# Performance work log

Hardware: AMD Instinct MI355X
Metric: run time of the kernel (lower is better)

Reference implementation:

```python
import jax, jax.numpy as jnp
import numpy as np

N = 100000      # nodes
E = 800000      # directed edges (self-loops added in reference, PyG default)
F_IN = 16
H1, C1 = 3, 32  # conv1: heads=3, out=32 (concat -> 96)
H2, C2 = 1, 32  # conv2: heads=1, out=32
NC = 16         # n_channel
SLOPE = 0.2     # PyG GATConv default negative_slope


def setup_inputs() -> dict:
    key = jax.random.key(0)
    ks = jax.random.split(key, 12)
    s = 0.1
    return {
        "x": jax.random.normal(ks[0], (N, F_IN), jnp.float32),
        "edge_index": jax.random.randint(ks[1], (2, E), 0, N, dtype=jnp.int32),
        "W1": jax.random.normal(ks[2], (F_IN, H1 * C1), jnp.float32) * s,
        "a_src1": jax.random.normal(ks[3], (H1, C1), jnp.float32) * s,
        "a_dst1": jax.random.normal(ks[4], (H1, C1), jnp.float32) * s,
        "b1": jnp.zeros((H1 * C1,), jnp.float32),
        "W2": jax.random.normal(ks[5], (H1 * C1, H2 * C2), jnp.float32) * s,
        "a_src2": jax.random.normal(ks[6], (H2, C2), jnp.float32) * s,
        "a_dst2": jax.random.normal(ks[7], (H2, C2), jnp.float32) * s,
        "b2": jnp.zeros((H2 * C2,), jnp.float32),
        "Wf": jax.random.normal(ks[8], (C2, NC), jnp.float32) * s,
        "bf": jnp.zeros((NC,), jnp.float32),
    }


def _gat_layer(x, src, dst, W, a_s, a_d, b, heads, outc):
    # x: [N, Fin]; src/dst: [Etot]
    h = (x @ W).reshape(N, heads, outc)                        # [N, H, C]
    alpha_s = (h * a_s).sum(-1)                                # [N, H]
    alpha_d = (h * a_d).sum(-1)                                # [N, H]
    e = jax.nn.leaky_relu(alpha_s[src] + alpha_d[dst], SLOPE)  # [Etot, H]
    # scatter-softmax over edges grouped by destination node
    m = jax.ops.segment_max(e, dst, num_segments=N)            # [N, H]
    p = jnp.exp(e - m[dst])
    z = jax.ops.segment_sum(p, dst, num_segments=N)
    alpha = p / (z[dst] + 1e-16)                               # [Etot, H]
    out = jax.ops.segment_sum(h[src] * alpha[:, :, None], dst, num_segments=N)
    return out.reshape(N, heads * outc) + b


def reference(x, edge_index, W1, a_src1, a_dst1, b1, W2, a_src2, a_dst2, b2, Wf, bf):
    loops = jnp.arange(N, dtype=edge_index.dtype)  # PyG add_self_loops=True
    src = jnp.concatenate([edge_index[0], loops])
    dst = jnp.concatenate([edge_index[1], loops])
    h = jax.nn.selu(_gat_layer(x, src, dst, W1, a_src1, a_dst1, b1, H1, C1))
    h = jax.nn.selu(_gat_layer(h, src, dst, W2, a_src2, a_dst2, b2, H2, C2))
    return h @ Wf + bf
```

## Files before the change

### kernel.cpp

```cpp
#include <hip/hip_runtime.h>
#include <hip/hip_bf16.h>

#define N_NODES 100000
#define N_EDGES 800000
#define F_IN    16
#define H1      3
#define C1      32
#define F1      (H1*C1)
#define F2      32
#define NC      16
#define SLOPE       0.2f
#define SELU_SCALE  1.0507009873554805f
#define SELU_ALPHA  1.6732632423543772f

#define DEG_PAD 48

#define NSLICE        8
#define BLK_PER_SLICE 256
#define SCAT_BLKS     (NSLICE * BLK_PER_SLICE)
#define EDGES_PER_BLK (N_EDGES / BLK_PER_SLICE)
#define SLICE_NODES   (N_NODES / NSLICE)
#define XB_NB   ((N_NODES + 255) / 256)

typedef unsigned short ushort_t;

__device__ __forceinline__ ushort_t f2bf(float f) {
    unsigned u = __float_as_uint(f);
    return (ushort_t)((u + 0x7FFFu + ((u >> 16) & 1u)) >> 16);
}
__device__ __forceinline__ unsigned pack2bf(float a, float b) {
    return (unsigned)f2bf(a) | ((unsigned)f2bf(b) << 16);
}
__device__ __forceinline__ float bf_lo(unsigned u) { return __uint_as_float(u << 16); }
__device__ __forceinline__ float bf_hi(unsigned u) { return __uint_as_float(u & 0xFFFF0000u); }

__device__ __forceinline__ void unpack8(const uint4 v, float* f) {
    f[0] = bf_lo(v.x); f[1] = bf_hi(v.x);
    f[2] = bf_lo(v.y); f[3] = bf_hi(v.y);
    f[4] = bf_lo(v.z); f[5] = bf_hi(v.z);
    f[6] = bf_lo(v.w); f[7] = bf_hi(v.w);
}
__device__ __forceinline__ float selu_f(float u) {
    return u > 0.f ? SELU_SCALE * u : SELU_SCALE * SELU_ALPHA * (__expf(u) - 1.f);
}

__global__ __launch_bounds__(256) void build_k(
    const int* __restrict__ ei, const float* __restrict__ x,
    const float* __restrict__ W1, const float* __restrict__ aS1,
    const float* __restrict__ aD1,
    int* __restrict__ deg, int* __restrict__ colp,
    uint4* __restrict__ xb, float4* __restrict__ as4, float4* __restrict__ ad4)
{
    __shared__ float swv[F_IN * 6];
    const int b = blockIdx.x, t = threadIdx.x;
    if (b < SCAT_BLKS) {
        const int slice = b & 7;
        const int lo = slice * SLICE_NODES, hi = lo + SLICE_NODES;
        const int e0 = (b >> 3) * EDGES_PER_BLK;
        for (int e = e0 + t; e < e0 + EDGES_PER_BLK; e += 256) {
            const int d = ei[N_EDGES + e];
            if (d >= lo && d < hi) {
                const int s = ei[e];
                const int pos = atomicAdd(&deg[d], 1);
                if (pos < DEG_PAD) colp[d * DEG_PAD + pos] = s;
            }
        }
    } else {
        if (t < 96) {
            const int k = t / 6, j = t % 6;
            const int h = (j < 3) ? j : j - 3;
            const float* a = (j < 3) ? aS1 : aD1;
            float acc = 0.f;
#pragma unroll
            for (int c = 0; c < 32; ++c) acc += W1[k * F1 + h * 32 + c] * a[h * 32 + c];
            swv[k * 6 + j] = acc;
        }
        __syncthreads();
        const int node = (b - SCAT_BLKS) * 256 + t;
        if (node < N_NODES) {
            float xr[16];
            const float4* xp = reinterpret_cast<const float4*>(&x[(size_t)node * F_IN]);
            const float4 v0 = xp[0], v1 = xp[1], v2 = xp[2], v3 = xp[3];
            xr[0] = v0.x; xr[1] = v0.y; xr[2]  = v0.z; xr[3]  = v0.w;
            xr[4] = v1.x; xr[5] = v1.y; xr[6]  = v1.z; xr[7]  = v1.w;
            xr[8] = v2.x; xr[9] = v2.y; xr[10] = v2.z; xr[11] = v2.w;
            xr[12] = v3.x; xr[13] = v3.y; xr[14] = v3.z; xr[15] = v3.w;
            uint4 o0, o1;
            o0.x = pack2bf(xr[0], xr[1]);   o0.y = pack2bf(xr[2], xr[3]);
            o0.z = pack2bf(xr[4], xr[5]);   o0.w = pack2bf(xr[6], xr[7]);
            o1.x = pack2bf(xr[8], xr[9]);   o1.y = pack2bf(xr[10], xr[11]);
            o1.z = pack2bf(xr[12], xr[13]); o1.w = pack2bf(xr[14], xr[15]);
            xb[(size_t)node * 2]     = o0;
            xb[(size_t)node * 2 + 1] = o1;
            float sacc[3] = {0.f, 0.f, 0.f}, dacc[3] = {0.f, 0.f, 0.f};
#pragma unroll
            for (int k = 0; k < 16; ++k) {
                const float xk = xr[k];
#pragma unroll
                for (int j = 0; j < 3; ++j) {
                    sacc[j] += xk * swv[k * 6 + j];
                    dacc[j] += xk * swv[k * 6 + 3 + j];
                }
            }
            as4[node] = make_float4(sacc[0], sacc[1], sacc[2], 0.f);
            ad4[node] = make_float4(dacc[0], dacc[1], dacc[2], 0.f);
        }
    }
}

__global__ __launch_bounds__(256) void agg1_k(
    const int* __restrict__ deg, const int* __restrict__ colp,
    const uint4* __restrict__ xb,
    const float4* __restrict__ as4, const float4* __restrict__ ad4,
    float* __restrict__ xagg)
{
    const int t = threadIdx.x;
    const int node = blockIdx.x * 64 + (t >> 2);
    const int u = t & 1;
    const int v = (t >> 1) & 1;
    if (node >= N_NODES) return;
    const int base = node * DEG_PAD;
    const int dg = min(deg[node], DEG_PAD);
    const float4 adv = ad4[node];

    float acc[3][8];
#pragma unroll
    for (int h = 0; h < 3; ++h)
#pragma unroll
        for (int i = 0; i < 8; ++i) acc[h][i] = 0.f;
    float z0 = 0.f, z1 = 0.f, z2 = 0.f;
    if (v == 0) {
        const float4 a = as4[node];
        float e0 = a.x + adv.x; e0 = e0 > 0.f ? e0 : SLOPE * e0;
        float e1 = a.y + adv.y; e1 = e1 > 0.f ? e1 : SLOPE * e1;
        float e2 = a.z + adv.z; e2 = e2 > 0.f ? e2 : SLOPE * e2;
        const float p0 = __expf(e0), p1 = __expf(e1), p2 = __expf(e2);
        z0 = p0; z1 = p1; z2 = p2;
        float xf[8]; unpack8(xb[(size_t)node * 2 + u], xf);
#pragma unroll
        for (int i = 0; i < 8; ++i) {
            acc[0][i] = p0 * xf[i]; acc[1][i] = p1 * xf[i]; acc[2][i] = p2 * xf[i];
        }
    }
    int j = v; uint4 hv; float4 av;
    if (j < dg) { const int s = colp[base + j]; av = as4[s]; hv = xb[(size_t)s * 2 + u]; }
    while (j < dg) {
        const uint4 cx = hv; const float4 ca = av;
        const int jn = j + 2;
        if (jn < dg) {
            const int s = colp[base + jn];
            av = as4[s]; hv = xb[(size_t)s * 2 + u];
        }
        float e0 = ca.x + adv.x; e0 = e0 > 0.f ? e0 : SLOPE * e0;
        float e1 = ca.y + adv.y; e1 = e1 > 0.f ? e1 : SLOPE * e1;
        float e2 = ca.z + adv.z; e2 = e2 > 0.f ? e2 : SLOPE * e2;
        const float p0 = __expf(e0), p1 = __expf(e1), p2 = __expf(e2);
        z0 += p0; z1 += p1; z2 += p2;
        float xf[8]; unpack8(cx, xf);
#pragma unroll
        for (int i = 0; i < 8; ++i) {
            acc[0][i] += p0 * xf[i]; acc[1][i] += p1 * xf[i]; acc[2][i] += p2 * xf[i];
        }
        j = jn;
    }
    z0 += __shfl_xor(z0, 2); z1 += __shfl_xor(z1, 2); z2 += __shfl_xor(z2, 2);
#pragma unroll
    for (int h = 0; h < 3; ++h)
#pragma unroll
        for (int i = 0; i < 8; ++i) acc[h][i] += __shfl_xor(acc[h][i], 2);
    if (v == 0) {
        const float zi[3] = {1.f / (z0 + 1e-16f), 1.f / (z1 + 1e-16f), 1.f / (z2 + 1e-16f)};
#pragma unroll
        for (int h = 0; h < 3; ++h) {
            float* dst = &xagg[(size_t)node * 48 + h * 16 + u * 8];
            *reinterpret_cast<float4*>(dst) =
                make_float4(acc[h][0] * zi[h], acc[h][1] * zi[h], acc[h][2] * zi[h], acc[h][3] * zi[h]);
            *reinterpret_cast<float4*>(dst + 4) =
                make_float4(acc[h][4] * zi[h], acc[h][5] * zi[h], acc[h][6] * zi[h], acc[h][7] * zi[h]);
        }
    }
}

__global__ __launch_bounds__(384) void l12_k(
    const float* __restrict__ xagg, const float* __restrict__ W1,
    const float* __restrict__ b1, const float* __restrict__ W2,
    const float* __restrict__ aS2, const float* __restrict__ aD2,
    ushort_t* __restrict__ h2b, float* __restrict__ as2, float* __restrict__ ad2)
{
    __shared__ float sW1[F_IN * F1];
    __shared__ float sxa[32 * 48];
    __shared__ float sx2[32][F1 + 1];
    __shared__ float sW2[F1 * F2];
    __shared__ float swv[F1 * 2];
    const int t = threadIdx.x;
    const int node0 = blockIdx.x * 32;

    {
        const float4 w = *reinterpret_cast<const float4*>(&W1[t * 4]);
        *reinterpret_cast<float4*>(&sW1[t * 4]) = w;
        const float4 xa = reinterpret_cast<const float4*>(xagg)[(size_t)node0 * 12 + t];
        *reinterpret_cast<float4*>(&sxa[t * 4]) = xa;
        const float4 w2a = *reinterpret_cast<const float4*>(&W2[t * 4]);
        *reinterpret_cast<float4*>(&sW2[t * 4]) = w2a;
        const float4 w2b = *reinterpret_cast<const float4*>(&W2[(t + 384) * 4]);
        *reinterpret_cast<float4*>(&sW2[(t + 384) * 4]) = w2b;
    }
    if (t < 192) {
        const int k = t >> 1, j = t & 1;
        const float* a = j ? aD2 : aS2;
        float acc = 0.f;
#pragma unroll
        for (int c = 0; c < 32; ++c) acc += W2[k * F2 + c] * a[c];
        swv[k * 2 + j] = acc;
    }
    __syncthreads();

    {
        const int c = t % 96;
        const int nloc = t / 96;
        const int hc = c >> 5;
        const float bc = b1[c];
#pragma unroll
        for (int g = 0; g < 8; ++g) {
            const int n = g * 4 + nloc;
            float acc = bc;
#pragma unroll
            for (int k = 0; k < F_IN; ++k) acc += sxa[n * 48 + hc * 16 + k] * sW1[k * F1 + c];
            sx2[n][c] = selu_f(acc);
        }
    }
    __syncthreads();

    if (t < 256) {
        const int nloc = t >> 3;
        const int cq = t & 7;
        float a0 = 0.f, a1 = 0.f, a2 = 0.f, a3 = 0.f;
#pragma unroll 8
        for (int k = 0; k < F1; ++k) {
            const float xk = sx2[nloc][k];
            const float4 w = *reinterpret_cast<const float4*>(&sW2[k * F2 + cq * 4]);
            a0 += xk * w.x; a1 += xk * w.y; a2 += xk * w.z; a3 += xk * w.w;
        }
        const int node = node0 + nloc;
        uint2 o;
        o.x = pack2bf(a0, a1); o.y = pack2bf(a2, a3);
        *reinterpret_cast<uint2*>(&h2b[(size_t)node * F2 + cq * 4]) = o;
        if (cq < 2) {
            float acc = 0.f;
#pragma unroll 8
            for (int k = 0; k < F1; ++k) acc += sx2[nloc][k] * swv[k * 2 + cq];
            if (cq == 0) as2[node] = acc;
            else         ad2[node] = acc;
        }
    }
}

__global__ __launch_bounds__(256) void agg2_final_k(
    const int* __restrict__ deg, const int* __restrict__ colp,
    const ushort_t* __restrict__ hb,
    const float* __restrict__ as, const float* __restrict__ ad,
    const float* __restrict__ b2, const float* __restrict__ Wf,
    const float* __restrict__ bf, float* __restrict__ out)
{
    __shared__ float sW[F2 * NC];
    __shared__ float sx[64][33];
    const int t = threadIdx.x;
    for (int i = t; i < F2 * NC; i += 256) sW[i] = Wf[i];
    const int sub = t >> 2;
    const int u = t & 1;
    const int v = (t >> 1) & 1;
    const int node = blockIdx.x * 64 + sub;
    const bool valid = node < N_NODES;

    if (valid) {
        const int base = node * DEG_PAD;
        const int dg = min(deg[node], DEG_PAD);
        const float adv = ad[node];
        float acc[16];
#pragma unroll
        for (int i = 0; i < 16; ++i) acc[i] = 0.f;
        float z = 0.f;
        if (v == 0) {
            float e = as[node] + adv; e = e > 0.f ? e : SLOPE * e;
            const float pv = __expf(e);
            z = pv;
            const uint4* hp = reinterpret_cast<const uint4*>(&hb[(size_t)node * F2 + u * 16]);
            float xf[8];
            unpack8(hp[0], xf);
#pragma unroll
            for (int i = 0; i < 8; ++i) acc[i] = pv * xf[i];
            unpack8(hp[1], xf);
#pragma unroll
            for (int i = 0; i < 8; ++i) acc[8 + i] = pv * xf[i];
        }
        int j = v; uint4 hva, hvb; float asv;
        if (j < dg) {
            const int s = colp[base + j];
            asv = as[s];
            const uint4* hp = reinterpret_cast<const uint4*>(&hb[(size_t)s * F2 + u * 16]);
            hva = hp[0]; hvb = hp[1];
        }
        while (j < dg) {
            const uint4 ca = hva, cb = hvb; const float cas = asv;
            const int jn = j + 2;
            if (jn < dg) {
                const int s = colp[base + jn];
                asv = as[s];
                const uint4* hp = reinterpret_cast<const uint4*>(&hb[(size_t)s * F2 + u * 16]);
                hva = hp[0]; hvb = hp[1];
            }
            float e = cas + adv; e = e > 0.f ? e : SLOPE * e;
            const float pv = __expf(e);
            z += pv;
            float xf[8];
            unpack8(ca, xf);
#pragma unroll
            for (int i = 0; i < 8; ++i) acc[i] += pv * xf[i];
            unpack8(cb, xf);
#pragma unroll
            for (int i = 0; i < 8; ++i) acc[8 + i] += pv * xf[i];
            j = jn;
        }
        z += __shfl_xor(z, 2);
#pragma unroll
        for (int i = 0; i < 16; ++i) acc[i] += __shfl_xor(acc[i], 2);
        if (v == 0) {
            const float zi = 1.f / (z + 1e-16f);
#pragma unroll
            for (int i = 0; i < 16; ++i)
                sx[sub][u * 16 + i] = selu_f(acc[i] * zi + b2[u * 16 + i]);
        }
    }
    __syncthreads();
    if (valid) {
        const int c0 = (t & 3) * 4;
        float r[4];
#pragma unroll
        for (int i = 0; i < 4; ++i) r[i] = bf[c0 + i];
#pragma unroll
        for (int k = 0; k < F2; ++k) {
            const float xk = sx[sub][k];
#pragma unroll
            for (int i = 0; i < 4; ++i) r[i] += xk * sW[k * NC + c0 + i];
        }
        *reinterpret_cast<float4*>(&out[(size_t)node * NC + c0]) =
            make_float4(r[0], r[1], r[2], r[3]);
    }
}

extern "C" void kernel_launch(void* const* d_in, const int* in_sizes, int n_in,
                              void* d_out, int out_size, void* d_ws, size_t ws_size,
                              hipStream_t stream)
{
    const float* x    = (const float*)d_in[0];
    const int*   ei   = (const int*)d_in[1];
    const float* W1   = (const float*)d_in[2];
    const float* aS1  = (const float*)d_in[3];
    const float* aD1  = (const float*)d_in[4];
    const float* b1   = (const float*)d_in[5];
    const float* W2   = (const float*)d_in[6];
    const float* aS2  = (const float*)d_in[7];
    const float* aD2  = (const float*)d_in[8];
    const float* b2   = (const float*)d_in[9];
    const float* Wf   = (const float*)d_in[10];
    const float* bf   = (const float*)d_in[11];
    float* out = (float*)d_out;

    uint4*    xb   = (uint4*)d_ws;
    float4*   as4  = (float4*)(xb + (size_t)N_NODES * 2);
    float4*   ad4  = as4 + N_NODES;
    float*    xagg = (float*)(ad4 + N_NODES);
    ushort_t* h2b  = (ushort_t*)(xagg + (size_t)N_NODES * 48);
    float*    as2  = (float*)(h2b + (size_t)N_NODES * F2);
    float*    ad2  = as2 + N_NODES;
    int*      colp = (int*)(ad2 + N_NODES);
    int*      deg  = colp + (size_t)N_NODES * DEG_PAD;

    hipMemsetAsync(deg, 0, sizeof(int) * N_NODES, stream);
    build_k<<<SCAT_BLKS + XB_NB, 256, 0, stream>>>(
        ei, x, W1, aS1, aD1, deg, colp, xb, as4, ad4);
    agg1_k<<<(N_NODES + 63) / 64, 256, 0, stream>>>(deg, colp, xb, as4, ad4, xagg);
    l12_k<<<N_NODES / 32, 384, 0, stream>>>(xagg, W1, b1, W2, aS2, aD2, h2b, as2, ad2);
    agg2_final_k<<<(N_NODES + 63) / 64, 256, 0, stream>>>(
        deg, colp, h2b, as2, ad2, b2, Wf, bf, out);
}
```

Baseline: 150.5 us.

## Transpose padded adjacency per slice, store xagg in bf16, retile l12 to 64 nodes

The padded neighbor list now uses a per-slice position-major layout, so adjacent destination nodes write and read neighbor slot j at adjacent addresses. The layer-1 aggregate is stored as bf16 instead of fp32, halving that intermediate's write and read traffic at some precision cost. The fused linear kernel now handles 64 nodes per block, with register-blocked weights and two nodes per thread, and gains bounds checks. The larger shared-memory tiles may reduce occupancy.

```diff
diff --git a/kernel.cpp b/kernel.cpp
--- a/kernel.cpp
+++ b/kernel.cpp
@@ -57,12 +57,13 @@
         const int slice = b & 7;
         const int lo = slice * SLICE_NODES, hi = lo + SLICE_NODES;
         const int e0 = (b >> 3) * EDGES_PER_BLK;
+        int* cslice = colp + (size_t)slice * DEG_PAD * SLICE_NODES;
         for (int e = e0 + t; e < e0 + EDGES_PER_BLK; e += 256) {
             const int d = ei[N_EDGES + e];
             if (d >= lo && d < hi) {
                 const int s = ei[e];
                 const int pos = atomicAdd(&deg[d], 1);
-                if (pos < DEG_PAD) colp[d * DEG_PAD + pos] = s;
+                if (pos < DEG_PAD) cslice[pos * SLICE_NODES + (d - lo)] = s;
             }
         }
     } else {
@@ -112,14 +113,16 @@
     const int* __restrict__ deg, const int* __restrict__ colp,
     const uint4* __restrict__ xb,
     const float4* __restrict__ as4, const float4* __restrict__ ad4,
-    float* __restrict__ xagg)
+    uint4* __restrict__ xagg_b)
 {
     const int t = threadIdx.x;
     const int node = blockIdx.x * 64 + (t >> 2);
     const int u = t & 1;
     const int v = (t >> 1) & 1;
     if (node >= N_NODES) return;
-    const int base = node * DEG_PAD;
+    const int slice = node / SLICE_NODES;
+    const int dl = node - slice * SLICE_NODES;
+    const int* cbase = colp + (size_t)slice * DEG_PAD * SLICE_NODES + dl;
     const int dg = min(deg[node], DEG_PAD);
     const float4 adv = ad4[node];
 
@@ -143,12 +146,12 @@
         }
     }
     int j = v; uint4 hv; float4 av;
-    if (j < dg) { const int s = colp[base + j]; av = as4[s]; hv = xb[(size_t)s * 2 + u]; }
+    if (j < dg) { const int s = cbase[j * SLICE_NODES]; av = as4[s]; hv = xb[(size_t)s * 2 + u]; }
     while (j < dg) {
         const uint4 cx = hv; const float4 ca = av;
         const int jn = j + 2;
         if (jn < dg) {
-            const int s = colp[base + jn];
+            const int s = cbase[jn * SLICE_NODES];
             av = as4[s]; hv = xb[(size_t)s * 2 + u];
         }
         float e0 = ca.x + adv.x; e0 = e0 > 0.f ? e0 : SLOPE * e0;
@@ -172,38 +175,43 @@
         const float zi[3] = {1.f / (z0 + 1e-16f), 1.f / (z1 + 1e-16f), 1.f / (z2 + 1e-16f)};
 #pragma unroll
         for (int h = 0; h < 3; ++h) {
-            float* dst = &xagg[(size_t)node * 48 + h * 16 + u * 8];
-            *reinterpret_cast<float4*>(dst) =
-                make_float4(acc[h][0] * zi[h], acc[h][1] * zi[h], acc[h][2] * zi[h], acc[h][3] * zi[h]);
-            *reinterpret_cast<float4*>(dst + 4) =
-                make_float4(acc[h][4] * zi[h], acc[h][5] * zi[h], acc[h][6] * zi[h], acc[h][7] * zi[h]);
+            uint4 o;
+            o.x = pack2bf(acc[h][0] * zi[h], acc[h][1] * zi[h]);
+            o.y = pack2bf(acc[h][2] * zi[h], acc[h][3] * zi[h]);
+            o.z = pack2bf(acc[h][4] * zi[h], acc[h][5] * zi[h]);
+            o.w = pack2bf(acc[h][6] * zi[h], acc[h][7] * zi[h]);
+            xagg_b[(size_t)node * 6 + h * 2 + u] = o;
         }
     }
 }
 
 __global__ __launch_bounds__(384) void l12_k(
-    const float* __restrict__ xagg, const float* __restrict__ W1,
+    const uint4* __restrict__ xagg_b, const float* __restrict__ W1,
     const float* __restrict__ b1, const float* __restrict__ W2,
     const float* __restrict__ aS2, const float* __restrict__ aD2,
     ushort_t* __restrict__ h2b, float* __restrict__ as2, float* __restrict__ ad2)
 {
     __shared__ float sW1[F_IN * F1];
-    __shared__ float sxa[32 * 48];
-    __shared__ float sx2[32][F1 + 1];
+    __shared__ float sxa[64 * 48];
+    __shared__ float sx2[64][F1 + 1];
     __shared__ float sW2[F1 * F2];
     __shared__ float swv[F1 * 2];
     const int t = threadIdx.x;
-    const int node0 = blockIdx.x * 32;
-
+    const int node0 = blockIdx.x * 64;
+
+    *reinterpret_cast<float4*>(&sW1[t * 4]) = *reinterpret_cast<const float4*>(&W1[t * 4]);
+    *reinterpret_cast<float4*>(&sW2[t * 4]) = *reinterpret_cast<const float4*>(&W2[t * 4]);
+    *reinterpret_cast<float4*>(&sW2[(t + 384) * 4]) =
+        *reinterpret_cast<const float4*>(&W2[(t + 384) * 4]);
     {
-        const float4 w = *reinterpret_cast<const float4*>(&W1[t * 4]);
-        *reinterpret_cast<float4*>(&sW1[t * 4]) = w;
-        const float4 xa = reinterpret_cast<const float4*>(xagg)[(size_t)node0 * 12 + t];
-        *reinterpret_cast<float4*>(&sxa[t * 4]) = xa;
-        const float4 w2a = *reinterpret_cast<const float4*>(&W2[t * 4]);
-        *reinterpret_cast<float4*>(&sW2[t * 4]) = w2a;
-        const float4 w2b = *reinterpret_cast<const float4*>(&W2[(t + 384) * 4]);
-        *reinterpret_cast<float4*>(&sW2[(t + 384) * 4]) = w2b;
+        const int nl = t / 6, w = t - nl * 6;
+        const int node = node0 + nl;
+        uint4 vv = make_uint4(0, 0, 0, 0);
+        if (node < N_NODES) vv = xagg_b[(size_t)node * 6 + w];
+        float xf[8]; unpack8(vv, xf);
+        float* dst = &sxa[nl * 48 + w * 8];
+        *reinterpret_cast<float4*>(dst)     = make_float4(xf[0], xf[1], xf[2], xf[3]);
+        *reinterpret_cast<float4*>(dst + 4) = make_float4(xf[4], xf[5], xf[6], xf[7]);
     }
     if (t < 192) {
         const int k = t >> 1, j = t & 1;
@@ -216,41 +224,64 @@
     __syncthreads();
 
     {
-        const int c = t % 96;
-        const int nloc = t / 96;
-        const int hc = c >> 5;
-        const float bc = b1[c];
-#pragma unroll
-        for (int g = 0; g < 8; ++g) {
-            const int n = g * 4 + nloc;
-            float acc = bc;
-#pragma unroll
-            for (int k = 0; k < F_IN; ++k) acc += sxa[n * 48 + hc * 16 + k] * sW1[k * F1 + c];
-            sx2[n][c] = selu_f(acc);
+        const int ng = t / 48;
+        const int cp = t - ng * 48;
+        const int c0 = cp * 2, c1 = c0 + 1;
+        const int hc = c0 >> 5;
+        float w0[16], w1[16];
+#pragma unroll
+        for (int k = 0; k < 16; ++k) { w0[k] = sW1[k * F1 + c0]; w1[k] = sW1[k * F1 + c1]; }
+        const float bc0 = b1[c0], bc1 = b1[c1];
+#pragma unroll
+        for (int nn = 0; nn < 8; ++nn) {
+            const int n = ng * 8 + nn;
+            const float4* xp = reinterpret_cast<const float4*>(&sxa[n * 48 + hc * 16]);
+            const float4 a0 = xp[0], a1 = xp[1], a2 = xp[2], a3 = xp[3];
+            const float xa[16] = {a0.x, a0.y, a0.z, a0.w, a1.x, a1.y, a1.z, a1.w,
+                                  a2.x, a2.y, a2.z, a2.w, a3.x, a3.y, a3.z, a3.w};
+            float acc0 = bc0, acc1 = bc1;
+#pragma unroll
+            for (int k = 0; k < 16; ++k) { acc0 += xa[k] * w0[k]; acc1 += xa[k] * w1[k]; }
+            sx2[n][c0] = selu_f(acc0);
+            sx2[n][c1] = selu_f(acc1);
         }
     }
     __syncthreads();
 
     if (t < 256) {
-        const int nloc = t >> 3;
         const int cq = t & 7;
-        float a0 = 0.f, a1 = 0.f, a2 = 0.f, a3 = 0.f;
-#pragma unroll 8
+        const int np = t >> 3;
+        const int n0 = np * 2, n1 = n0 + 1;
+        float acc0[4] = {0.f, 0.f, 0.f, 0.f}, acc1[4] = {0.f, 0.f, 0.f, 0.f};
+#pragma unroll 4
         for (int k = 0; k < F1; ++k) {
-            const float xk = sx2[nloc][k];
             const float4 w = *reinterpret_cast<const float4*>(&sW2[k * F2 + cq * 4]);
-            a0 += xk * w.x; a1 += xk * w.y; a2 += xk * w.z; a3 += xk * w.w;
-        }
-        const int node = node0 + nloc;
-        uint2 o;
-        o.x = pack2bf(a0, a1); o.y = pack2bf(a2, a3);
-        *reinterpret_cast<uint2*>(&h2b[(size_t)node * F2 + cq * 4]) = o;
+            const float x0 = sx2[n0][k], x1 = sx2[n1][k];
+            acc0[0] += x0 * w.x; acc0[1] += x0 * w.y; acc0[2] += x0 * w.z; acc0[3] += x0 * w.w;
+            acc1[0] += x1 * w.x; acc1[1] += x1 * w.y; acc1[2] += x1 * w.z; acc1[3] += x1 * w.w;
+        }
+        if (node0 + n0 < N_NODES) {
+            uint2 o; o.x = pack2bf(acc0[0], acc0[1]); o.y = pack2bf(acc0[2], acc0[3]);
+            *reinterpret_cast<uint2*>(&h2b[(size_t)(node0 + n0) * F2 + cq * 4]) = o;
+        }
+        if (node0 + n1 < N_NODES) {
+            uint2 o; o.x = pack2bf(acc1[0], acc1[1]); o.y = pack2bf(acc1[2], acc1[3]);
+            *reinterpret_cast<uint2*>(&h2b[(size_t)(node0 + n1) * F2 + cq * 4]) = o;
+        }
         if (cq < 2) {
-            float acc = 0.f;
-#pragma unroll 8
-            for (int k = 0; k < F1; ++k) acc += sx2[nloc][k] * swv[k * 2 + cq];
-            if (cq == 0) as2[node] = acc;
-            else         ad2[node] = acc;
+            float s0 = 0.f, s1 = 0.f;
+#pragma unroll 4
+            for (int k = 0; k < F1; ++k) {
+                const float wv = swv[k * 2 + cq];
+                s0 += sx2[n0][k] * wv; s1 += sx2[n1][k] * wv;
+            }
+            if (cq == 0) {
+                if (node0 + n0 < N_NODES) as2[node0 + n0] = s0;
+                if (node0 + n1 < N_NODES) as2[node0 + n1] = s1;
+            } else {
+                if (node0 + n0 < N_NODES) ad2[node0 + n0] = s0;
+                if (node0 + n1 < N_NODES) ad2[node0 + n1] = s1;
+            }
         }
     }
 }
@@ -273,7 +304,9 @@
     const bool valid = node < N_NODES;
 
     if (valid) {
-        const int base = node * DEG_PAD;
+        const int slice = node / SLICE_NODES;
+        const int dl = node - slice * SLICE_NODES;
+        const int* cbase = colp + (size_t)slice * DEG_PAD * SLICE_NODES + dl;
         const int dg = min(deg[node], DEG_PAD);
         const float adv = ad[node];
         float acc[16];
@@ -295,7 +328,7 @@
         }
         int j = v; uint4 hva, hvb; float asv;
         if (j < dg) {
-            const int s = colp[base + j];
+            const int s = cbase[j * SLICE_NODES];
             asv = as[s];
             const uint4* hp = reinterpret_cast<const uint4*>(&hb[(size_t)s * F2 + u * 16]);
             hva = hp[0]; hvb = hp[1];
@@ -304,7 +337,7 @@
             const uint4 ca = hva, cb = hvb; const float cas = asv;
             const int jn = j + 2;
             if (jn < dg) {
-                const int s = colp[base + jn];
+                const int s = cbase[jn * SLICE_NODES];
                 asv = as[s];
                 const uint4* hp = reinterpret_cast<const uint4*>(&hb[(size_t)s * F2 + u * 16]);
                 hva = hp[0]; hvb = hp[1];
@@ -366,21 +399,22 @@
     const float* bf   = (const float*)d_in[11];
     float* out = (float*)d_out;
 
-    uint4*    xb   = (uint4*)d_ws;
-    float4*   as4  = (float4*)(xb + (size_t)N_NODES * 2);
-    float4*   ad4  = as4 + N_NODES;
-    float*    xagg = (float*)(ad4 + N_NODES);
-    ushort_t* h2b  = (ushort_t*)(xagg + (size_t)N_NODES * 48);
-    float*    as2  = (float*)(h2b + (size_t)N_NODES * F2);
-    float*    ad2  = as2 + N_NODES;
-    int*      colp = (int*)(ad2 + N_NODES);
-    int*      deg  = colp + (size_t)N_NODES * DEG_PAD;
+    uint4*    xb     = (uint4*)d_ws;
+    float4*   as4    = (float4*)(xb + (size_t)N_NODES * 2);
+    float4*   ad4    = as4 + N_NODES;
+    uint4*    xagg_b = (uint4*)(ad4 + N_NODES);
+    ushort_t* h2b    = (ushort_t*)(xagg_b + (size_t)N_NODES * 6);
+    float*    as2    = (float*)(h2b + (size_t)N_NODES * F2);
+    float*    ad2    = as2 + N_NODES;
+    int*      colp   = (int*)(ad2 + N_NODES);
+    int*      deg    = colp + (size_t)N_NODES * DEG_PAD;
 
     hipMemsetAsync(deg, 0, sizeof(int) * N_NODES, stream);
     build_k<<<SCAT_BLKS + XB_NB, 256, 0, stream>>>(
         ei, x, W1, aS1, aD1, deg, colp, xb, as4, ad4);
-    agg1_k<<<(N_NODES + 63) / 64, 256, 0, stream>>>(deg, colp, xb, as4, ad4, xagg);
-    l12_k<<<N_NODES / 32, 384, 0, stream>>>(xagg, W1, b1, W2, aS2, aD2, h2b, as2, ad2);
+    agg1_k<<<(N_NODES + 63) / 64, 256, 0, stream>>>(deg, colp, xb, as4, ad4, xagg_b);
+    l12_k<<<(N_NODES + 63) / 64, 384, 0, stream>>>(
+        xagg_b, W1, b1, W2, aS2, aD2, h2b, as2, ad2);
     agg2_final_k<<<(N_NODES + 63) / 64, 256, 0, stream>>>(
         deg, colp, h2b, as2, ad2, b2, Wf, bf, out);
 }
```

Result: faster. 141.2 us (-6.2%).
